# Kernel optimization log

Measured on AMD Instinct MI355X. Metric: run time of the kernel, lower is better.

## Reference

```python
import jax, jax.numpy as jnp
import numpy as np

B, N, F = 4, 4096, 6
K = 8
EPS = 1e-3  # keras BatchNormalization default epsilon


def _dense_params(key, fan_in, fan_out):
    lim = np.sqrt(6.0 / (fan_in + fan_out))
    w = jax.random.uniform(key, (fan_in, fan_out), jnp.float32, -lim, lim)
    return w, jnp.zeros((fan_out,), jnp.float32)


def setup_inputs() -> dict:
    key = jax.random.key(0)
    ks = jax.random.split(key, 12)
    inp = {}
    inp["inputs"] = jax.random.normal(ks[0], (B, N, F), jnp.float32)
    # BatchNorm 1 (over F channels), inference-mode moving stats
    inp["bn1_gamma"] = jnp.ones((F,), jnp.float32)
    inp["bn1_beta"] = jnp.zeros((F,), jnp.float32)
    inp["bn1_mean"] = jnp.zeros((F,), jnp.float32)
    inp["bn1_var"] = jnp.ones((F,), jnp.float32)
    # GravNet1 MLP: Dense(F-2 -> 32, relu), Dense(32 -> 32)
    inp["g1_w1"], inp["g1_b1"] = _dense_params(ks[1], F - 2, 32)
    inp["g1_w2"], inp["g1_b2"] = _dense_params(ks[2], 32, 32)
    # GravNet2 MLP: Dense(32 -> 32, relu), Dense(32 -> 32)
    inp["g2_w1"], inp["g2_b1"] = _dense_params(ks[3], 32, 32)
    inp["g2_w2"], inp["g2_b2"] = _dense_params(ks[4], 32, 32)
    # trailing dense stack: concat(x1, x2) has dim 34+34 = 68
    inp["d1_w"], inp["d1_b"] = _dense_params(ks[5], 68, 128)
    inp["d2_w"], inp["d2_b"] = _dense_params(ks[6], 128, 64)
    inp["d3_w"], inp["d3_b"] = _dense_params(ks[7], 64, 32)
    inp["bn2_gamma"] = jnp.ones((32,), jnp.float32)
    inp["bn2_beta"] = jnp.zeros((32,), jnp.float32)
    inp["bn2_mean"] = jnp.zeros((32,), jnp.float32)
    inp["bn2_var"] = jnp.ones((32,), jnp.float32)
    inp["out_w"], inp["out_b"] = _dense_params(ks[8], 32, 1)
    return inp


def _batchnorm(x, gamma, beta, mean, var):
    return (x - mean) * jax.lax.rsqrt(var + EPS) * gamma + beta


def _gravnet(x, w1, b1, w2, b2):
    pos, feat = x[..., :2], x[..., 2:]              # [B,N,2], [B,N,Fd]
    diff = pos[:, :, None, :] - pos[:, None, :, :]  # [B,N,N,2]
    d2 = jnp.sum(diff * diff, axis=-1)              # squared dist: same ordering as tf.norm
    _, idx = jax.lax.top_k(-d2, K + 1)              # ascending-distance indices
    idx = idx[..., 1:]                              # drop self -> [B,N,K]
    nb = jax.vmap(lambda f, i: f[i])(feat, idx)     # gather, batch_dims=1 -> [B,N,K,Fd]
    agg = jnp.mean(nb, axis=-2)                     # [B,N,Fd]
    h = jax.nn.relu(agg @ w1 + b1) @ w2 + b2        # MLP -> [B,N,32]
    return jnp.concatenate([pos, h], axis=-1)       # [B,N,34]


def reference(inputs, bn1_gamma, bn1_beta, bn1_mean, bn1_var,
              g1_w1, g1_b1, g1_w2, g1_b2,
              g2_w1, g2_b1, g2_w2, g2_b2,
              d1_w, d1_b, d2_w, d2_b, d3_w, d3_b,
              bn2_gamma, bn2_beta, bn2_mean, bn2_var,
              out_w, out_b):
    x = _batchnorm(inputs, bn1_gamma, bn1_beta, bn1_mean, bn1_var)
    x1 = _gravnet(x, g1_w1, g1_b1, g1_w2, g1_b2)
    x2 = _gravnet(x1, g2_w1, g2_b1, g2_w2, g2_b2)
    x = jnp.concatenate([x1, x2], axis=-1)          # [B,N,68]
    x = jax.nn.relu(x @ d1_w + d1_b)
    x = jax.nn.relu(x @ d2_w + d2_b)
    x = jax.nn.relu(x @ d3_w + d3_b)
    x = _batchnorm(x, bn2_gamma, bn2_beta, bn2_mean, bn2_var)
    return x @ out_w + out_b                        # [B,N,1]
```

## Files before the change

### kernel.cpp

```cpp
#include <hip/hip_runtime.h>
#include <hip/hip_bf16.h>

#define BTOT 4
#define NPTS 4096
#define FTOT 6
#define KNN 8
#define EPSV 1e-3f

template <int P>
__device__ __forceinline__ unsigned long long swz_xor_u64(unsigned long long v) {
    unsigned lo = (unsigned)v, hi = (unsigned)(v >> 32);
    lo = (unsigned)__builtin_amdgcn_ds_swizzle((int)lo, P);
    hi = (unsigned)__builtin_amdgcn_ds_swizzle((int)hi, P);
    return ((unsigned long long)hi << 32) | lo;
}
#define MERGE_STEP(P) { unsigned long long o_ = swz_xor_u64<P>(mn); mn = (o_ < mn) ? o_ : mn; }
#define MERGE_MIN_U64_32() \
    MERGE_STEP(0x041F) MERGE_STEP(0x081F) MERGE_STEP(0x101F) MERGE_STEP(0x201F) MERGE_STEP(0x401F)

__global__ __launch_bounds__(256) void k_bn1(const float* __restrict__ in,
                                             const float* __restrict__ g,
                                             const float* __restrict__ b,
                                             const float* __restrict__ m,
                                             const float* __restrict__ v,
                                             float* __restrict__ x,
                                             float2* __restrict__ pos) {
    int i = blockIdx.x * 256 + threadIdx.x;
    if (i >= BTOT * NPTS) return;
    float o[FTOT];
#pragma unroll
    for (int f = 0; f < FTOT; ++f) {
        float val = in[(size_t)i * FTOT + f];
        o[f] = (val - m[f]) * rsqrtf(v[f] + EPSV) * g[f] + b[f];
        x[(size_t)i * FTOT + f] = o[f];
    }
    pos[i] = make_float2(o[0], o[1]);
}

__global__ __launch_bounds__(512) void k_knn(const float2* __restrict__ posg,
                                             int* __restrict__ idx) {
    __shared__ float2 spos[NPTS];
    int b  = blockIdx.x >> 8;
    int q0 = (blockIdx.x & 255) << 4;
    int t  = threadIdx.x;
    const float2* pb = posg + (size_t)b * NPTS;
    for (int j = t; j < NPTS; j += 512) spos[j] = pb[j];
    __syncthreads();

    int lq = t >> 5;
    int p  = t & 31;
    int qq = q0 + lq;
    float2 q = spos[qq];

    unsigned long long bm0 = ~0ULL, bm1 = ~0ULL, bm2 = ~0ULL, bm3 = ~0ULL;
    for (int jj = 0; jj < NPTS / 32; jj += 4) {
        int j0 = ((jj + 0) << 5) + p;
        int j1 = ((jj + 1) << 5) + p;
        int j2 = ((jj + 2) << 5) + p;
        int j3 = ((jj + 3) << 5) + p;
        float2 p0 = spos[j0], p1 = spos[j1], p2 = spos[j2], p3 = spos[j3];
        float d0 = __fadd_rn(__fmul_rn(q.x - p0.x, q.x - p0.x), __fmul_rn(q.y - p0.y, q.y - p0.y));
        float d1 = __fadd_rn(__fmul_rn(q.x - p1.x, q.x - p1.x), __fmul_rn(q.y - p1.y, q.y - p1.y));
        float d2 = __fadd_rn(__fmul_rn(q.x - p2.x, q.x - p2.x), __fmul_rn(q.y - p2.y, q.y - p2.y));
        float d3 = __fadd_rn(__fmul_rn(q.x - p3.x, q.x - p3.x), __fmul_rn(q.y - p3.y, q.y - p3.y));
        unsigned long long k0 = ((unsigned long long)__float_as_uint(d0) << 32) | (unsigned)j0;
        unsigned long long k1 = ((unsigned long long)__float_as_uint(d1) << 32) | (unsigned)j1;
        unsigned long long k2 = ((unsigned long long)__float_as_uint(d2) << 32) | (unsigned)j2;
        unsigned long long k3 = ((unsigned long long)__float_as_uint(d3) << 32) | (unsigned)j3;
        bm0 = k0 < bm0 ? k0 : bm0;
        bm1 = k1 < bm1 ? k1 : bm1;
        bm2 = k2 < bm2 ? k2 : bm2;
        bm3 = k3 < bm3 ? k3 : bm3;
    }
    unsigned long long bma = bm0 < bm1 ? bm0 : bm1;
    unsigned long long bmb = bm2 < bm3 ? bm2 : bm3;
    unsigned long long bm  = bma < bmb ? bma : bmb;

    unsigned long long KK = bm, r = 0;
#pragma unroll
    for (int rd = 0; rd < 9; ++rd) {
        unsigned long long mn = KK;
        MERGE_MIN_U64_32()
        if (KK == mn) KK = ~0ULL;
        r = mn;
    }
    unsigned long long sent = r + 1;

    unsigned long long K[9];
#pragma unroll
    for (int m = 0; m < 9; ++m) K[m] = sent;

#pragma unroll 4
    for (int jj = 0; jj < NPTS / 32; ++jj) {
        int j = (jj << 5) + p;
        float2 pt = spos[j];
        float dx = q.x - pt.x;
        float dy = q.y - pt.y;
        float d2 = __fadd_rn(__fmul_rn(dx, dx), __fmul_rn(dy, dy));
        unsigned long long key = ((unsigned long long)__float_as_uint(d2) << 32) | (unsigned)j;
        if (key < K[8]) {
            K[8] = key;
#pragma unroll
            for (int m = 8; m > 0; --m) {
                bool sw = K[m] < K[m - 1];
                unsigned long long a = sw ? K[m - 1] : K[m];
                unsigned long long c = sw ? K[m] : K[m - 1];
                K[m] = a; K[m - 1] = c;
            }
        }
    }

    int rec = qq;
#pragma unroll
    for (int rd = 0; rd < 9; ++rd) {
        unsigned long long mn = K[0];
        MERGE_MIN_U64_32()
        if (K[0] == mn) {
#pragma unroll
            for (int i = 0; i < 8; ++i) K[i] = K[i + 1];
            K[8] = ~0ULL;
        }
        if (rd >= 1 && p == rd - 1) rec = (int)(unsigned)mn;
    }
    rec &= (NPTS - 1);
    if (p < 8)
        idx[((size_t)b * NPTS + qq) * KNN + p] = rec;
}

__global__ __launch_bounds__(256) void k_g1(const float* __restrict__ x,
                                            const int* __restrict__ idx,
                                            const float* __restrict__ w1,
                                            const float* __restrict__ b1,
                                            const float* __restrict__ w2,
                                            const float* __restrict__ b2,
                                            float* __restrict__ xcat) {
    __shared__ float sw1[4 * 33], sw2[32 * 33], sb1[32], sb2[32];
    int t = threadIdx.x;
    if (t < 128) sw1[(t >> 5) * 33 + (t & 31)] = w1[t];
    for (int u = t; u < 1024; u += 256) sw2[(u >> 5) * 33 + (u & 31)] = w2[u];
    if (t < 32) { sb1[t] = b1[t]; sb2[t] = b2[t]; }
    __syncthreads();

    int i = blockIdx.x * 64 + (t >> 2);
    int s = t & 3;
    int qb = (t & 63) & ~3;
    int b = i >> 12;
    int n = i & (NPTS - 1);
    const float* xb = x + (size_t)b * NPTS * FTOT;

    float aggs = 0.f;
#pragma unroll
    for (int k = 0; k < KNN; ++k) {
        int nb = idx[(size_t)i * KNN + k];
        aggs += xb[(size_t)nb * FTOT + 2 + s];
    }
    aggs *= 0.125f;

    float af0 = __shfl(aggs, qb + 0);
    float af1 = __shfl(aggs, qb + 1);
    float af2 = __shfl(aggs, qb + 2);
    float af3 = __shfl(aggs, qb + 3);

    int o0 = 8 * s;
    float h[8];
#pragma unroll
    for (int u = 0; u < 8; ++u) {
        int o = o0 + u;
        float a = af0 * sw1[0 * 33 + o] + af1 * sw1[1 * 33 + o]
                + af2 * sw1[2 * 33 + o] + af3 * sw1[3 * 33 + o];
        h[u] = fmaxf(a + sb1[o], 0.f);
    }

    float hf[32];
#pragma unroll
    for (int w = 0; w < 4; ++w)
#pragma unroll
        for (int u = 0; u < 8; ++u)
            hf[8 * w + u] = __shfl(h[u], qb + w);

    float* oc = xcat + (size_t)i * 68;
    if (s == 0) {
        oc[0] = xb[(size_t)n * FTOT];
        oc[1] = xb[(size_t)n * FTOT + 1];
    }
#pragma unroll
    for (int u = 0; u < 8; ++u) {
        int o = o0 + u;
        float a = 0.f;
#pragma unroll
        for (int k = 0; k < 32; ++k) a += hf[k] * sw2[k * 33 + o];
        oc[2 + o] = a + sb2[o];
    }
}

__global__ __launch_bounds__(256) void k_g2(float* __restrict__ xcat,
                                            const int* __restrict__ idx,
                                            const float* __restrict__ w1,
                                            const float* __restrict__ b1,
                                            const float* __restrict__ w2,
                                            const float* __restrict__ b2) {
    __shared__ float sw1[32 * 33], sw2[32 * 33], sb1[32], sb2[32];
    int t = threadIdx.x;
    for (int u = t; u < 1024; u += 256) {
        sw1[(u >> 5) * 33 + (u & 31)] = w1[u];
        sw2[(u >> 5) * 33 + (u & 31)] = w2[u];
    }
    if (t < 32) { sb1[t] = b1[t]; sb2[t] = b2[t]; }
    __syncthreads();

    int i = blockIdx.x * 64 + (t >> 2);
    int s = t & 3;
    int qb = (t & 63) & ~3;
    int b = i >> 12;

    float agg[8];
#pragma unroll
    for (int u = 0; u < 8; ++u) agg[u] = 0.f;
#pragma unroll
    for (int k = 0; k < KNN; ++k) {
        int nb = idx[(size_t)i * KNN + k];
        const float2* f2 = (const float2*)(xcat + ((size_t)b * NPTS + nb) * 68 + 2 + 8 * s);
#pragma unroll
        for (int w = 0; w < 4; ++w) {
            float2 a = f2[w];
            agg[2 * w]     += a.x;
            agg[2 * w + 1] += a.y;
        }
    }
#pragma unroll
    for (int u = 0; u < 8; ++u) agg[u] *= 0.125f;

    float af[32];
#pragma unroll
    for (int w = 0; w < 4; ++w)
#pragma unroll
        for (int u = 0; u < 8; ++u)
            af[8 * w + u] = __shfl(agg[u], qb + w);

    int o0 = 8 * s;
    float h[8];
#pragma unroll
    for (int u = 0; u < 8; ++u) {
        int o = o0 + u;
        float a = 0.f;
#pragma unroll
        for (int k = 0; k < 32; ++k) a += af[k] * sw1[k * 33 + o];
        h[u] = fmaxf(a + sb1[o], 0.f);
    }

    float hf[32];
#pragma unroll
    for (int w = 0; w < 4; ++w)
#pragma unroll
        for (int u = 0; u < 8; ++u)
            hf[8 * w + u] = __shfl(h[u], qb + w);

    float* oc = xcat + (size_t)i * 68;
    if (s == 0) {
        oc[34] = oc[0];
        oc[35] = oc[1];
    }
#pragma unroll
    for (int u = 0; u < 8; ++u) {
        int o = o0 + u;
        float a = 0.f;
#pragma unroll
        for (int k = 0; k < 32; ++k) a += hf[k] * sw2[k * 33 + o];
        oc[36 + o] = a + sb2[o];
    }
}

__global__ __launch_bounds__(256) void k_mlp(const float* __restrict__ xcat,
                                             const float* __restrict__ w1, const float* __restrict__ b1,
                                             const float* __restrict__ w2, const float* __restrict__ b2,
                                             const float* __restrict__ w3, const float* __restrict__ b3,
                                             const float* __restrict__ g,  const float* __restrict__ be,
                                             const float* __restrict__ mn, const float* __restrict__ vr,
                                             const float* __restrict__ ow, const float* __restrict__ ob,
                                             float* __restrict__ out) {
    __shared__ float xT[68][36];
    __shared__ float h1T[128][36];
    __shared__ float h2T[64][36];
    int t = threadIdx.x;
    int base = blockIdx.x * 32;

    for (int u = t; u < 32 * 68; u += 256) {
        int p = u / 68, k = u - p * 68;
        xT[k][p] = xcat[(size_t)(base + p) * 68 + k];
    }
    __syncthreads();

    int pq = t & 7;
    int oq = t >> 3;

    {
        float4 bb = *(const float4*)(b1 + 4 * oq);
        float4 a0 = make_float4(bb.x, bb.x, bb.x, bb.x);
        float4 a1 = make_float4(bb.y, bb.y, bb.y, bb.y);
        float4 a2 = make_float4(bb.z, bb.z, bb.z, bb.z);
        float4 a3 = make_float4(bb.w, bb.w, bb.w, bb.w);
#pragma unroll 4
        for (int k = 0; k < 68; ++k) {
            float4 xv = *(const float4*)&xT[k][4 * pq];
            float4 wv = *(const float4*)(w1 + (size_t)k * 128 + 4 * oq);
            a0.x += wv.x * xv.x; a0.y += wv.x * xv.y; a0.z += wv.x * xv.z; a0.w += wv.x * xv.w;
            a1.x += wv.y * xv.x; a1.y += wv.y * xv.y; a1.z += wv.y * xv.z; a1.w += wv.y * xv.w;
            a2.x += wv.z * xv.x; a2.y += wv.z * xv.y; a2.z += wv.z * xv.z; a2.w += wv.z * xv.w;
            a3.x += wv.w * xv.x; a3.y += wv.w * xv.y; a3.z += wv.w * xv.z; a3.w += wv.w * xv.w;
        }
        a0.x = fmaxf(a0.x, 0.f); a0.y = fmaxf(a0.y, 0.f); a0.z = fmaxf(a0.z, 0.f); a0.w = fmaxf(a0.w, 0.f);
        a1.x = fmaxf(a1.x, 0.f); a1.y = fmaxf(a1.y, 0.f); a1.z = fmaxf(a1.z, 0.f); a1.w = fmaxf(a1.w, 0.f);
        a2.x = fmaxf(a2.x, 0.f); a2.y = fmaxf(a2.y, 0.f); a2.z = fmaxf(a2.z, 0.f); a2.w = fmaxf(a2.w, 0.f);
        a3.x = fmaxf(a3.x, 0.f); a3.y = fmaxf(a3.y, 0.f); a3.z = fmaxf(a3.z, 0.f); a3.w = fmaxf(a3.w, 0.f);
        *(float4*)&h1T[4 * oq + 0][4 * pq] = a0;
        *(float4*)&h1T[4 * oq + 1][4 * pq] = a1;
        *(float4*)&h1T[4 * oq + 2][4 * pq] = a2;
        *(float4*)&h1T[4 * oq + 3][4 * pq] = a3;
    }
    __syncthreads();

    if (t < 128) {
        float4 bb = *(const float4*)(b2 + 4 * oq);
        float4 a0 = make_float4(bb.x, bb.x, bb.x, bb.x);
        float4 a1 = make_float4(bb.y, bb.y, bb.y, bb.y);
        float4 a2 = make_float4(bb.z, bb.z, bb.z, bb.z);
        float4 a3 = make_float4(bb.w, bb.w, bb.w, bb.w);
#pragma unroll 4
        for (int k = 0; k < 128; ++k) {
            float4 xv = *(const float4*)&h1T[k][4 * pq];
            float4 wv = *(const float4*)(w2 + (size_t)k * 64 + 4 * oq);
            a0.x += wv.x * xv.x; a0.y += wv.x * xv.y; a0.z += wv.x * xv.z; a0.w += wv.x * xv.w;
            a1.x += wv.y * xv.x; a1.y += wv.y * xv.y; a1.z += wv.y * xv.z; a1.w += wv.y * xv.w;
            a2.x += wv.z * xv.x; a2.y += wv.z * xv.y; a2.z += wv.z * xv.z; a2.w += wv.z * xv.w;
            a3.x += wv.w * xv.x; a3.y += wv.w * xv.y; a3.z += wv.w * xv.z; a3.w += wv.w * xv.w;
        }
        a0.x = fmaxf(a0.x, 0.f); a0.y = fmaxf(a0.y, 0.f); a0.z = fmaxf(a0.z, 0.f); a0.w = fmaxf(a0.w, 0.f);
        a1.x = fmaxf(a1.x, 0.f); a1.y = fmaxf(a1.y, 0.f); a1.z = fmaxf(a1.z, 0.f); a1.w = fmaxf(a1.w, 0.f);
        a2.x = fmaxf(a2.x, 0.f); a2.y = fmaxf(a2.y, 0.f); a2.z = fmaxf(a2.z, 0.f); a2.w = fmaxf(a2.w, 0.f);
        a3.x = fmaxf(a3.x, 0.f); a3.y = fmaxf(a3.y, 0.f); a3.z = fmaxf(a3.z, 0.f); a3.w = fmaxf(a3.w, 0.f);
        *(float4*)&h2T[4 * oq + 0][4 * pq] = a0;
        *(float4*)&h2T[4 * oq + 1][4 * pq] = a1;
        *(float4*)&h2T[4 * oq + 2][4 * pq] = a2;
        *(float4*)&h2T[4 * oq + 3][4 * pq] = a3;
    }
    __syncthreads();

    if (t < 64) {
        float4 bb = *(const float4*)(b3 + 4 * oq);
        float4 a0 = make_float4(bb.x, bb.x, bb.x, bb.x);
        float4 a1 = make_float4(bb.y, bb.y, bb.y, bb.y);
        float4 a2 = make_float4(bb.z, bb.z, bb.z, bb.z);
        float4 a3 = make_float4(bb.w, bb.w, bb.w, bb.w);
#pragma unroll 4
        for (int k = 0; k < 64; ++k) {
            float4 xv = *(const float4*)&h2T[k][4 * pq];
            float4 wv = *(const float4*)(w3 + (size_t)k * 32 + 4 * oq);
            a0.x += wv.x * xv.x; a0.y += wv.x * xv.y; a0.z += wv.x * xv.z; a0.w += wv.x * xv.w;
            a1.x += wv.y * xv.x; a1.y += wv.y * xv.y; a1.z += wv.y * xv.z; a1.w += wv.y * xv.w;
            a2.x += wv.z * xv.x; a2.y += wv.z * xv.y; a2.z += wv.z * xv.z; a2.w += wv.z * xv.w;
            a3.x += wv.w * xv.x; a3.y += wv.w * xv.y; a3.z += wv.w * xv.z; a3.w += wv.w * xv.w;
        }
        a0.x = fmaxf(a0.x, 0.f); a0.y = fmaxf(a0.y, 0.f); a0.z = fmaxf(a0.z, 0.f); a0.w = fmaxf(a0.w, 0.f);
        a1.x = fmaxf(a1.x, 0.f); a1.y = fmaxf(a1.y, 0.f); a1.z = fmaxf(a1.z, 0.f); a1.w = fmaxf(a1.w, 0.f);
        a2.x = fmaxf(a2.x, 0.f); a2.y = fmaxf(a2.y, 0.f); a2.z = fmaxf(a2.z, 0.f); a2.w = fmaxf(a2.w, 0.f);
        a3.x = fmaxf(a3.x, 0.f); a3.y = fmaxf(a3.y, 0.f); a3.z = fmaxf(a3.z, 0.f); a3.w = fmaxf(a3.w, 0.f);
        int c0 = 4 * oq;
        float s0 = g[c0 + 0] * rsqrtf(vr[c0 + 0] + EPSV);
        float s1 = g[c0 + 1] * rsqrtf(vr[c0 + 1] + EPSV);
        float s2 = g[c0 + 2] * rsqrtf(vr[c0 + 2] + EPSV);
        float s3 = g[c0 + 3] * rsqrtf(vr[c0 + 3] + EPSV);
        float w0 = s0 * ow[c0 + 0], w1c = s1 * ow[c0 + 1];
        float w2c = s2 * ow[c0 + 2], w3c = s3 * ow[c0 + 3];
        float tt = (be[c0 + 0] - mn[c0 + 0] * s0) * ow[c0 + 0]
                 + (be[c0 + 1] - mn[c0 + 1] * s1) * ow[c0 + 1]
                 + (be[c0 + 2] - mn[c0 + 2] * s2) * ow[c0 + 2]
                 + (be[c0 + 3] - mn[c0 + 3] * s3) * ow[c0 + 3];
        float4 s;
        s.x = a0.x * w0 + a1.x * w1c + a2.x * w2c + a3.x * w3c;
        s.y = a0.y * w0 + a1.y * w1c + a2.y * w2c + a3.y * w3c;
        s.z = a0.z * w0 + a1.z * w1c + a2.z * w2c + a3.z * w3c;
        s.w = a0.w * w0 + a1.w * w1c + a2.w * w2c + a3.w * w3c;
#pragma unroll
        for (int msk = 8; msk <= 32; msk <<= 1) {
            s.x += __shfl_xor(s.x, msk);
            s.y += __shfl_xor(s.y, msk);
            s.z += __shfl_xor(s.z, msk);
            s.w += __shfl_xor(s.w, msk);
            tt  += __shfl_xor(tt,  msk);
        }
        if (oq == 0) {
            float c = tt + ob[0];
            *(float4*)(out + base + 4 * pq) = make_float4(s.x + c, s.y + c, s.z + c, s.w + c);
        }
    }
}

extern "C" void kernel_launch(void* const* d_in, const int* in_sizes, int n_in,
                              void* d_out, int out_size, void* d_ws, size_t ws_size,
                              hipStream_t stream) {
    const float* inputs    = (const float*)d_in[0];
    const float* bn1_gamma = (const float*)d_in[1];
    const float* bn1_beta  = (const float*)d_in[2];
    const float* bn1_mean  = (const float*)d_in[3];
    const float* bn1_var   = (const float*)d_in[4];
    const float* g1_w1 = (const float*)d_in[5];
    const float* g1_b1 = (const float*)d_in[6];
    const float* g1_w2 = (const float*)d_in[7];
    const float* g1_b2 = (const float*)d_in[8];
    const float* g2_w1 = (const float*)d_in[9];
    const float* g2_b1 = (const float*)d_in[10];
    const float* g2_w2 = (const float*)d_in[11];
    const float* g2_b2 = (const float*)d_in[12];
    const float* d1_w = (const float*)d_in[13];
    const float* d1_b = (const float*)d_in[14];
    const float* d2_w = (const float*)d_in[15];
    const float* d2_b = (const float*)d_in[16];
    const float* d3_w = (const float*)d_in[17];
    const float* d3_b = (const float*)d_in[18];
    const float* bn2_gamma = (const float*)d_in[19];
    const float* bn2_beta  = (const float*)d_in[20];
    const float* bn2_mean  = (const float*)d_in[21];
    const float* bn2_var   = (const float*)d_in[22];
    const float* out_w = (const float*)d_in[23];
    const float* out_b = (const float*)d_in[24];
    float* out = (float*)d_out;

    const size_t BN = (size_t)BTOT * NPTS;
    char* ws = (char*)d_ws;
    size_t off = 0;
    auto alloc = [&](size_t bytes) { char* p = ws + off; off += (bytes + 255) & ~(size_t)255; return p; };
    float*  x    = (float*) alloc(BN * FTOT * sizeof(float));
    float2* pos  = (float2*)alloc(BN * sizeof(float2));
    int*    idx  = (int*)   alloc(BN * KNN  * sizeof(int));
    float*  xcat = (float*) alloc(BN * 68   * sizeof(float));
    (void)ws_size; (void)n_in; (void)in_sizes; (void)out_size;

    k_bn1<<<dim3(64),   dim3(256), 0, stream>>>(inputs, bn1_gamma, bn1_beta, bn1_mean, bn1_var, x, pos);
    k_knn<<<dim3(1024), dim3(512), 0, stream>>>(pos, idx);
    k_g1 <<<dim3(256),  dim3(256), 0, stream>>>(x, idx, g1_w1, g1_b1, g1_w2, g1_b2, xcat);
    k_g2 <<<dim3(256),  dim3(256), 0, stream>>>(xcat, idx, g2_w1, g2_b1, g2_w2, g2_b2);
    k_mlp<<<dim3(512),  dim3(256), 0, stream>>>(xcat, d1_w, d1_b, d2_w, d2_b, d3_w, d3_b,
                                                bn2_gamma, bn2_beta, bn2_mean, bn2_var,
                                                out_w, out_b, out);
}
```

Before: 101.4 us.

## Fuse second GravNet layer into trailing MLP kernel via shared memory

Merges the second GravNet kernel into the dense-stack kernel. Each 32-point block now computes the neighbour aggregation and the GravNet2 MLP, writing x2 straight into the shared transposed tile instead of back to global xcat. This removes one kernel launch and a global write and re-read of the x2 half of xcat. The cost is that only 128 of 256 threads work during the GravNet phase, and the kernel uses more shared memory, which may reduce occupancy.

```diff
diff --git a/kernel.cpp b/kernel.cpp
--- a/kernel.cpp
+++ b/kernel.cpp
@@ -193,84 +193,10 @@
     }
 }
 
-__global__ __launch_bounds__(256) void k_g2(float* __restrict__ xcat,
-                                            const int* __restrict__ idx,
-                                            const float* __restrict__ w1,
-                                            const float* __restrict__ b1,
-                                            const float* __restrict__ w2,
-                                            const float* __restrict__ b2) {
-    __shared__ float sw1[32 * 33], sw2[32 * 33], sb1[32], sb2[32];
-    int t = threadIdx.x;
-    for (int u = t; u < 1024; u += 256) {
-        sw1[(u >> 5) * 33 + (u & 31)] = w1[u];
-        sw2[(u >> 5) * 33 + (u & 31)] = w2[u];
-    }
-    if (t < 32) { sb1[t] = b1[t]; sb2[t] = b2[t]; }
-    __syncthreads();
-
-    int i = blockIdx.x * 64 + (t >> 2);
-    int s = t & 3;
-    int qb = (t & 63) & ~3;
-    int b = i >> 12;
-
-    float agg[8];
-#pragma unroll
-    for (int u = 0; u < 8; ++u) agg[u] = 0.f;
-#pragma unroll
-    for (int k = 0; k < KNN; ++k) {
-        int nb = idx[(size_t)i * KNN + k];
-        const float2* f2 = (const float2*)(xcat + ((size_t)b * NPTS + nb) * 68 + 2 + 8 * s);
-#pragma unroll
-        for (int w = 0; w < 4; ++w) {
-            float2 a = f2[w];
-            agg[2 * w]     += a.x;
-            agg[2 * w + 1] += a.y;
-        }
-    }
-#pragma unroll
-    for (int u = 0; u < 8; ++u) agg[u] *= 0.125f;
-
-    float af[32];
-#pragma unroll
-    for (int w = 0; w < 4; ++w)
-#pragma unroll
-        for (int u = 0; u < 8; ++u)
-            af[8 * w + u] = __shfl(agg[u], qb + w);
-
-    int o0 = 8 * s;
-    float h[8];
-#pragma unroll
-    for (int u = 0; u < 8; ++u) {
-        int o = o0 + u;
-        float a = 0.f;
-#pragma unroll
-        for (int k = 0; k < 32; ++k) a += af[k] * sw1[k * 33 + o];
-        h[u] = fmaxf(a + sb1[o], 0.f);
-    }
-
-    float hf[32];
-#pragma unroll
-    for (int w = 0; w < 4; ++w)
-#pragma unroll
-        for (int u = 0; u < 8; ++u)
-            hf[8 * w + u] = __shfl(h[u], qb + w);
-
-    float* oc = xcat + (size_t)i * 68;
-    if (s == 0) {
-        oc[34] = oc[0];
-        oc[35] = oc[1];
-    }
-#pragma unroll
-    for (int u = 0; u < 8; ++u) {
-        int o = o0 + u;
-        float a = 0.f;
-#pragma unroll
-        for (int k = 0; k < 32; ++k) a += hf[k] * sw2[k * 33 + o];
-        oc[36 + o] = a + sb2[o];
-    }
-}
-
-__global__ __launch_bounds__(256) void k_mlp(const float* __restrict__ xcat,
+__global__ __launch_bounds__(256) void k_g2m(const float* __restrict__ xcat,
+                                             const int* __restrict__ idx,
+                                             const float* __restrict__ gw1, const float* __restrict__ gb1,
+                                             const float* __restrict__ gw2, const float* __restrict__ gb2,
                                              const float* __restrict__ w1, const float* __restrict__ b1,
                                              const float* __restrict__ w2, const float* __restrict__ b2,
                                              const float* __restrict__ w3, const float* __restrict__ b3,
@@ -278,15 +204,85 @@
                                              const float* __restrict__ mn, const float* __restrict__ vr,
                                              const float* __restrict__ ow, const float* __restrict__ ob,
                                              float* __restrict__ out) {
+    __shared__ float sw1[32 * 33], sw2[32 * 33], sb1[32], sb2[32];
     __shared__ float xT[68][36];
     __shared__ float h1T[128][36];
     __shared__ float h2T[64][36];
     int t = threadIdx.x;
     int base = blockIdx.x * 32;
 
-    for (int u = t; u < 32 * 68; u += 256) {
-        int p = u / 68, k = u - p * 68;
+    for (int u = t; u < 1024; u += 256) {
+        sw1[(u >> 5) * 33 + (u & 31)] = gw1[u];
+        sw2[(u >> 5) * 33 + (u & 31)] = gw2[u];
+    }
+    if (t < 32) { sb1[t] = gb1[t]; sb2[t] = gb2[t]; }
+    for (int u = t; u < 32 * 34; u += 256) {
+        int p = u / 34, k = u - p * 34;
         xT[k][p] = xcat[(size_t)(base + p) * 68 + k];
+    }
+    __syncthreads();
+
+    if (t < 128) {
+        int pt = t >> 2;
+        int s  = t & 3;
+        int qb = (t & 63) & ~3;
+        int i  = base + pt;
+        int b  = i >> 12;
+
+        float agg[8];
+#pragma unroll
+        for (int u = 0; u < 8; ++u) agg[u] = 0.f;
+#pragma unroll
+        for (int k = 0; k < KNN; ++k) {
+            int nb = idx[(size_t)i * KNN + k];
+            const float2* f2 = (const float2*)(xcat + ((size_t)b * NPTS + nb) * 68 + 2 + 8 * s);
+#pragma unroll
+            for (int w = 0; w < 4; ++w) {
+                float2 a = f2[w];
+                agg[2 * w]     += a.x;
+                agg[2 * w + 1] += a.y;
+            }
+        }
+#pragma unroll
+        for (int u = 0; u < 8; ++u) agg[u] *= 0.125f;
+
+        float af[32];
+#pragma unroll
+        for (int w = 0; w < 4; ++w)
+#pragma unroll
+            for (int u = 0; u < 8; ++u)
+                af[8 * w + u] = __shfl(agg[u], qb + w);
+
+        int o0 = 8 * s;
+        float h[8];
+#pragma unroll
+        for (int u = 0; u < 8; ++u) {
+            int o = o0 + u;
+            float a = 0.f;
+#pragma unroll
+            for (int k = 0; k < 32; ++k) a += af[k] * sw1[k * 33 + o];
+            h[u] = fmaxf(a + sb1[o], 0.f);
+        }
+
+        float hf[32];
+#pragma unroll
+        for (int w = 0; w < 4; ++w)
+#pragma unroll
+            for (int u = 0; u < 8; ++u)
+                hf[8 * w + u] = __shfl(h[u], qb + w);
+
+        if (s == 0) {
+            xT[34][pt] = xT[0][pt];
+            xT[35][pt] = xT[1][pt];
+        }
+#pragma unroll
+        for (int u = 0; u < 8; ++u) {
+            int o = o0 + u;
+            float a = 0.f;
+#pragma unroll
+            for (int k = 0; k < 32; ++k) a += hf[k] * sw2[k * 33 + o];
+            xT[36 + o][pt] = a + sb2[o];
+        }
     }
     __syncthreads();
 
@@ -438,8 +434,9 @@
     k_bn1<<<dim3(64),   dim3(256), 0, stream>>>(inputs, bn1_gamma, bn1_beta, bn1_mean, bn1_var, x, pos);
     k_knn<<<dim3(1024), dim3(512), 0, stream>>>(pos, idx);
     k_g1 <<<dim3(256),  dim3(256), 0, stream>>>(x, idx, g1_w1, g1_b1, g1_w2, g1_b2, xcat);
-    k_g2 <<<dim3(256),  dim3(256), 0, stream>>>(xcat, idx, g2_w1, g2_b1, g2_w2, g2_b2);
-    k_mlp<<<dim3(512),  dim3(256), 0, stream>>>(xcat, d1_w, d1_b, d2_w, d2_b, d3_w, d3_b,
+    k_g2m<<<dim3(512),  dim3(256), 0, stream>>>(xcat, idx,
+                                                g2_w1, g2_b1, g2_w2, g2_b2,
+                                                d1_w, d1_b, d2_w, d2_b, d3_w, d3_b,
                                                 bn2_gamma, bn2_beta, bn2_mean, bn2_var,
                                                 out_w, out_b, out);
 }
```

Result: faster. 97.21 us (median of 2 runs) (-4.1%).
